# Kernel tuning notes

Measured on AMD Instinct MI355X. Metric: run time of the kernel, lower is better.

## Reference

```python
import jax, jax.numpy as jnp
import numpy as np

BETA = 0.25  # commitment_cost
K = 512      # num_embeddings
D = 64       # embedding_dim


def setup_inputs() -> dict:
    key = jax.random.key(0)
    k1, k2 = jax.random.split(key)
    z = jax.random.normal(k1, (8, D, 16, 64, 64), dtype=jnp.float32)
    # torch init: uniform_(-1/K, 1/K)
    emb = jax.random.uniform(k2, (K, D), dtype=jnp.float32,
                             minval=-1.0 / K, maxval=1.0 / K)
    return {"z": z, "emb": emb}


def reference(z, emb):
    B, Dc, d, h, w = z.shape
    # (B, D, d, h, w) -> (N, D), N = B*d*h*w
    z_flat = jnp.transpose(z, (0, 2, 3, 4, 1)).reshape(-1, Dc)
    # squared euclidean distances to each codebook entry: (N, K)
    dists = (jnp.sum(z_flat * z_flat, axis=1, keepdims=True)
             - 2.0 * (z_flat @ emb.T)
             + jnp.sum(emb * emb, axis=1))
    indices = jnp.argmin(dists, axis=1)                      # (N,)
    z_q = emb[indices]                                       # (N, D) gather
    z_q = jnp.transpose(z_q.reshape(B, d, h, w, Dc), (0, 4, 1, 2, 3))
    codebook_loss = jnp.mean((z_q - jax.lax.stop_gradient(z)) ** 2)
    commitment_loss = jnp.mean((jax.lax.stop_gradient(z_q) - z) ** 2)
    loss = codebook_loss + BETA * commitment_loss
    # straight-through estimator
    z_q_st = z + jax.lax.stop_gradient(z_q - z)
    return (z_q_st, loss, indices.reshape(B, d, h, w))
```

## Files before the change

### kernel.cpp

```cpp
#include <hip/hip_runtime.h>


#define NK       512
#define DD       64
#define LOSS_OFF 33554432
#define IDX_OFF  33554433
#define EE_FOFF  4

typedef float f32x4 __attribute__((ext_vector_type(4)));

__device__ __forceinline__ float np_sumsq64(const float* v) {
#pragma clang fp contract(off)
    float r[8];
    #pragma unroll
    for (int j = 0; j < 8; ++j) {
        float s = v[j] * v[j];
        r[j] = s;
    }
    #pragma unroll
    for (int i = 8; i < 64; i += 8) {
        #pragma unroll
        for (int j = 0; j < 8; ++j) {
            float s = v[i + j] * v[i + j];
            r[j] += s;
        }
    }
    return ((r[0] + r[1]) + (r[2] + r[3])) + ((r[4] + r[5]) + (r[6] + r[7]));
}

__global__ void vq_ee(const float* __restrict__ emb, float* __restrict__ ws) {
    const int k = blockIdx.x * 256 + threadIdx.x;
    if (blockIdx.x == 0 && threadIdx.x == 0) {
        ((double*)ws)[0] = 0.0;
        ((double*)ws)[1] = 0.0;
    }
    float row[DD];
    const float* er = emb + k * DD;
    #pragma unroll
    for (int c = 0; c < DD; ++c) row[c] = er[c];
    ws[EE_FOFF + k] = np_sumsq64(row);
}

__global__ __launch_bounds__(256)
__attribute__((amdgpu_waves_per_eu(3, 3)))
void vq_main(const float* __restrict__ z, const float* __restrict__ emb,
             float* __restrict__ out, float* __restrict__ ws) {
    __shared__ f32x4 elds[2048];
    __shared__ float eelds[NK];

    const int tid = threadIdx.x;
    const int n0  = blockIdx.x * 512 + tid;
    const int n1  = n0 + 256;
    const int b   = n0 >> 16;
    const int sp  = n0 & 65535;
    const float* zp0 = z + ((size_t)b << 22) + sp;
    const float* zp1 = zp0 + 256;

    eelds[tid]       = ws[EE_FOFF + tid];
    eelds[tid + 256] = ws[EE_FOFF + tid + 256];

    float za[DD], zb[DD];
    #pragma unroll
    for (int c = 0; c < DD; ++c) za[c] = zp0[(size_t)c << 16];
    #pragma unroll
    for (int c = 0; c < DD; ++c) zb[c] = zp1[(size_t)c << 16];
    const float zz0 = np_sumsq64(za);
    const float zz1 = np_sumsq64(zb);

    const f32x4* eg = (const f32x4*)emb;

    float best0 = 3.4e38f, best1 = 3.4e38f;
    int   bi0   = 0,        bi1   = 0;

    #pragma unroll 1
    for (int p = 0; p < 4; ++p) {
        __syncthreads();
        #pragma unroll
        for (int r = 0; r < 8; ++r)
            elds[r * 256 + tid] = eg[p * 2048 + r * 256 + tid];
        __syncthreads();

        #pragma unroll 1
        for (int kl = 0; kl < 128; ++kl) {
            float m0 = 0.f, m1 = 0.f;
            #pragma unroll
            for (int c4 = 0; c4 < 16; ++c4) {
                const f32x4 e = elds[kl * 16 + c4];
                const int c = c4 * 4;
                m0 = fmaf(za[c + 0], e.x, m0);  m1 = fmaf(zb[c + 0], e.x, m1);
                m0 = fmaf(za[c + 1], e.y, m0);  m1 = fmaf(zb[c + 1], e.y, m1);
                m0 = fmaf(za[c + 2], e.z, m0);  m1 = fmaf(zb[c + 2], e.z, m1);
                m0 = fmaf(za[c + 3], e.w, m0);  m1 = fmaf(zb[c + 3], e.w, m1);
            }
            const int k = p * 128 + kl;
            const float ee = eelds[k];
            const float d0 = fmaf(-2.f, m0, zz0) + ee;
            const float d1 = fmaf(-2.f, m1, zz1) + ee;
            if (d0 < best0) { best0 = d0; bi0 = k; }
            if (d1 < best1) { best1 = d1; bi1 = k; }
        }
    }

    float* op0 = out + ((size_t)b << 22) + sp;
    float* op1 = op0 + 256;
    const float4* br0 = (const float4*)(emb + bi0 * DD);
    const float4* br1 = (const float4*)(emb + bi1 * DD);
    float lsum = 0.f;
    #pragma unroll
    for (int c4 = 0; c4 < 16; ++c4) {
        float4 e0 = br0[c4];
        float4 e1 = br1[c4];
        float eq0[4] = { e0.x, e0.y, e0.z, e0.w };
        float eq1[4] = { e1.x, e1.y, e1.z, e1.w };
        #pragma unroll
        for (int j = 0; j < 4; ++j) {
            const int c = c4 * 4 + j;
            float da = eq0[j] - za[c];
            float db = eq1[j] - zb[c];
            lsum = fmaf(da, da, lsum);
            lsum = fmaf(db, db, lsum);
            op0[(size_t)c << 16] = eq0[j];
            op1[(size_t)c << 16] = eq1[j];
        }
    }
    out[IDX_OFF + n0] = (float)bi0;
    out[IDX_OFF + n1] = (float)bi1;

    #pragma unroll
    for (int off = 32; off > 0; off >>= 1) lsum += __shfl_down(lsum, off);
    if ((tid & 63) == 0)
        atomicAdd((double*)ws, (double)lsum);
}

__global__ void vq_finalize(const float* __restrict__ ws, float* __restrict__ out) {
    out[LOSS_OFF] = (float)(((const double*)ws)[0] * (1.25 / 33554432.0));
}

extern "C" void kernel_launch(void* const* d_in, const int* in_sizes, int n_in,
                              void* d_out, int out_size, void* d_ws, size_t ws_size,
                              hipStream_t stream) {
    const float* z   = (const float*)d_in[0];
    const float* emb = (const float*)d_in[1];
    float* out = (float*)d_out;
    float* ws  = (float*)d_ws;

    vq_ee<<<dim3(2), dim3(256), 0, stream>>>(emb, ws);
    vq_main<<<dim3(1024), dim3(256), 0, stream>>>(z, emb, out, ws);
    vq_finalize<<<dim3(1), dim3(1), 0, stream>>>(ws, out);
}
```

Baseline: 730.3 us.

## Process four rows per thread to increase codebook reuse from LDS

Each thread now holds four z rows in registers instead of two and computes distances for all four against each codebook entry read from shared memory, halving LDS reads per FMA. The codebook norms are read as float4 once per four entries. The grid is halved, and the occupancy hint drops to one wave per EU to allow the much larger register footprint. This trades latency hiding and occupancy for fewer shared-memory loads.

```diff
diff --git a/kernel.cpp b/kernel.cpp
--- a/kernel.cpp
+++ b/kernel.cpp
@@ -42,35 +42,35 @@
 }
 
 __global__ __launch_bounds__(256)
-__attribute__((amdgpu_waves_per_eu(3, 3)))
+__attribute__((amdgpu_waves_per_eu(1, 1)))
 void vq_main(const float* __restrict__ z, const float* __restrict__ emb,
              float* __restrict__ out, float* __restrict__ ws) {
     __shared__ f32x4 elds[2048];
-    __shared__ float eelds[NK];
+    __shared__ f32x4 eelds4[128];
 
     const int tid = threadIdx.x;
-    const int n0  = blockIdx.x * 512 + tid;
-    const int n1  = n0 + 256;
-    const int b   = n0 >> 16;
-    const int sp  = n0 & 65535;
-    const float* zp0 = z + ((size_t)b << 22) + sp;
-    const float* zp1 = zp0 + 256;
+    const int blk = blockIdx.x;
+    const int b   = blk >> 6;
+    const int sp0 = (blk & 63) * 1024 + tid;
+    const float* zb = z + ((size_t)b << 22);
 
-    eelds[tid]       = ws[EE_FOFF + tid];
-    eelds[tid + 256] = ws[EE_FOFF + tid + 256];
+    if (tid < 128)
+        eelds4[tid] = ((const f32x4*)(ws + EE_FOFF))[tid];
 
-    float za[DD], zb[DD];
+    float zr[4][DD];
     #pragma unroll
-    for (int c = 0; c < DD; ++c) za[c] = zp0[(size_t)c << 16];
+    for (int j = 0; j < 4; ++j)
+        #pragma unroll
+        for (int c = 0; c < DD; ++c)
+            zr[j][c] = zb[sp0 + j * 256 + ((size_t)c << 16)];
+    float zz[4];
     #pragma unroll
-    for (int c = 0; c < DD; ++c) zb[c] = zp1[(size_t)c << 16];
-    const float zz0 = np_sumsq64(za);
-    const float zz1 = np_sumsq64(zb);
+    for (int j = 0; j < 4; ++j) zz[j] = np_sumsq64(zr[j]);
 
     const f32x4* eg = (const f32x4*)emb;
 
-    float best0 = 3.4e38f, best1 = 3.4e38f;
-    int   bi0   = 0,        bi1   = 0;
+    float best0 = 3.4e38f, best1 = 3.4e38f, best2 = 3.4e38f, best3 = 3.4e38f;
+    int   bi0 = 0, bi1 = 0, bi2 = 0, bi3 = 0;
 
     #pragma unroll 1
     for (int p = 0; p < 4; ++p) {
@@ -81,50 +81,61 @@
         __syncthreads();
 
         #pragma unroll 1
-        for (int kl = 0; kl < 128; ++kl) {
-            float m0 = 0.f, m1 = 0.f;
+        for (int ko = 0; ko < 32; ++ko) {
+            const f32x4 ee4 = eelds4[p * 32 + ko];
             #pragma unroll
-            for (int c4 = 0; c4 < 16; ++c4) {
-                const f32x4 e = elds[kl * 16 + c4];
-                const int c = c4 * 4;
-                m0 = fmaf(za[c + 0], e.x, m0);  m1 = fmaf(zb[c + 0], e.x, m1);
-                m0 = fmaf(za[c + 1], e.y, m0);  m1 = fmaf(zb[c + 1], e.y, m1);
-                m0 = fmaf(za[c + 2], e.z, m0);  m1 = fmaf(zb[c + 2], e.z, m1);
-                m0 = fmaf(za[c + 3], e.w, m0);  m1 = fmaf(zb[c + 3], e.w, m1);
+            for (int ki = 0; ki < 4; ++ki) {
+                const int kl = ko * 4 + ki;
+                float m0 = 0.f, m1 = 0.f, m2 = 0.f, m3 = 0.f;
+                #pragma unroll
+                for (int c4 = 0; c4 < 16; ++c4) {
+                    const f32x4 e = elds[kl * 16 + c4];
+                    const int c = c4 * 4;
+                    m0 = fmaf(zr[0][c+0], e.x, m0); m1 = fmaf(zr[1][c+0], e.x, m1);
+                    m2 = fmaf(zr[2][c+0], e.x, m2); m3 = fmaf(zr[3][c+0], e.x, m3);
+                    m0 = fmaf(zr[0][c+1], e.y, m0); m1 = fmaf(zr[1][c+1], e.y, m1);
+                    m2 = fmaf(zr[2][c+1], e.y, m2); m3 = fmaf(zr[3][c+1], e.y, m3);
+                    m0 = fmaf(zr[0][c+2], e.z, m0); m1 = fmaf(zr[1][c+2], e.z, m1);
+                    m2 = fmaf(zr[2][c+2], e.z, m2); m3 = fmaf(zr[3][c+2], e.z, m3);
+                    m0 = fmaf(zr[0][c+3], e.w, m0); m1 = fmaf(zr[1][c+3], e.w, m1);
+                    m2 = fmaf(zr[2][c+3], e.w, m2); m3 = fmaf(zr[3][c+3], e.w, m3);
+                }
+                const int k = p * 128 + kl;
+                const float ee = (ki == 0) ? ee4.x : (ki == 1) ? ee4.y
+                               : (ki == 2) ? ee4.z : ee4.w;
+                const float d0 = fmaf(-2.f, m0, zz[0]) + ee;
+                const float d1 = fmaf(-2.f, m1, zz[1]) + ee;
+                const float d2 = fmaf(-2.f, m2, zz[2]) + ee;
+                const float d3 = fmaf(-2.f, m3, zz[3]) + ee;
+                if (d0 < best0) { best0 = d0; bi0 = k; }
+                if (d1 < best1) { best1 = d1; bi1 = k; }
+                if (d2 < best2) { best2 = d2; bi2 = k; }
+                if (d3 < best3) { best3 = d3; bi3 = k; }
             }
-            const int k = p * 128 + kl;
-            const float ee = eelds[k];
-            const float d0 = fmaf(-2.f, m0, zz0) + ee;
-            const float d1 = fmaf(-2.f, m1, zz1) + ee;
-            if (d0 < best0) { best0 = d0; bi0 = k; }
-            if (d1 < best1) { best1 = d1; bi1 = k; }
         }
     }
 
-    float* op0 = out + ((size_t)b << 22) + sp;
-    float* op1 = op0 + 256;
-    const float4* br0 = (const float4*)(emb + bi0 * DD);
-    const float4* br1 = (const float4*)(emb + bi1 * DD);
+    float* ob = out + ((size_t)b << 22);
+    const int bis[4] = { bi0, bi1, bi2, bi3 };
     float lsum = 0.f;
     #pragma unroll
-    for (int c4 = 0; c4 < 16; ++c4) {
-        float4 e0 = br0[c4];
-        float4 e1 = br1[c4];
-        float eq0[4] = { e0.x, e0.y, e0.z, e0.w };
-        float eq1[4] = { e1.x, e1.y, e1.z, e1.w };
+    for (int j = 0; j < 4; ++j) {
+        float* op = ob + sp0 + j * 256;
+        const float4* brow = (const float4*)(emb + bis[j] * DD);
         #pragma unroll
-        for (int j = 0; j < 4; ++j) {
-            const int c = c4 * 4 + j;
-            float da = eq0[j] - za[c];
-            float db = eq1[j] - zb[c];
-            lsum = fmaf(da, da, lsum);
-            lsum = fmaf(db, db, lsum);
-            op0[(size_t)c << 16] = eq0[j];
-            op1[(size_t)c << 16] = eq1[j];
+        for (int c4 = 0; c4 < 16; ++c4) {
+            float4 e = brow[c4];
+            float eq[4] = { e.x, e.y, e.z, e.w };
+            #pragma unroll
+            for (int q = 0; q < 4; ++q) {
+                const int c = c4 * 4 + q;
+                float dd = eq[q] - zr[j][c];
+                lsum = fmaf(dd, dd, lsum);
+                op[(size_t)c << 16] = eq[q];
+            }
         }
+        out[IDX_OFF + ((size_t)b << 16) + sp0 + j * 256] = (float)bis[j];
     }
-    out[IDX_OFF + n0] = (float)bi0;
-    out[IDX_OFF + n1] = (float)bi1;
 
     #pragma unroll
     for (int off = 32; off > 0; off >>= 1) lsum += __shfl_down(lsum, off);
@@ -145,6 +156,6 @@
     float* ws  = (float*)d_ws;
 
     vq_ee<<<dim3(2), dim3(256), 0, stream>>>(emb, ws);
-    vq_main<<<dim3(1024), dim3(256), 0, stream>>>(z, emb, out, ws);
+    vq_main<<<dim3(512), dim3(256), 0, stream>>>(z, emb, out, ws);
     vq_finalize<<<dim3(1), dim3(1), 0, stream>>>(ws, out);
 }
```

Result: slower. 1.061 ms (+45.3%).

## Pack two rows into f32x2 FMAs and split codebook reads between LDS and global

Applied to the files above, without the earlier changes.

Stores the two per-thread z vectors interleaved as f32x2 so the inner distance loop can use packed FMA on two rows at once. Only the first quarter of each codebook row (16 of 64 dims) goes into LDS; the rest is read through uniform global/scalar loads, and the row norms are read from the workspace per pair of codes. This removes the per-phase LDS reloads and barriers. It also lowers waves_per_eu from 3 to 2 to free registers. The change depends on the compiler emitting packed FP32 ops and on the global codebook reads staying cache-resident. The near-tie argmin order could shift slightly with fp contract off.

```diff
diff --git a/kernel.cpp b/kernel.cpp
--- a/kernel.cpp
+++ b/kernel.cpp
@@ -7,6 +7,7 @@
 #define IDX_OFF  33554433
 #define EE_FOFF  4
 
+typedef float f32x2 __attribute__((ext_vector_type(2)));
 typedef float f32x4 __attribute__((ext_vector_type(4)));
 
 __device__ __forceinline__ float np_sumsq64(const float* v) {
@@ -42,11 +43,11 @@
 }
 
 __global__ __launch_bounds__(256)
-__attribute__((amdgpu_waves_per_eu(3, 3)))
+__attribute__((amdgpu_waves_per_eu(2, 2)))
 void vq_main(const float* __restrict__ z, const float* __restrict__ emb,
              float* __restrict__ out, float* __restrict__ ws) {
-    __shared__ f32x4 elds[2048];
-    __shared__ float eelds[NK];
+#pragma clang fp contract(off)
+    __shared__ f32x4 elds[NK * 4];
 
     const int tid = threadIdx.x;
     const int n0  = blockIdx.x * 512 + tid;
@@ -56,48 +57,79 @@
     const float* zp0 = z + ((size_t)b << 22) + sp;
     const float* zp1 = zp0 + 256;
 
-    eelds[tid]       = ws[EE_FOFF + tid];
-    eelds[tid + 256] = ws[EE_FOFF + tid + 256];
+    const f32x4* eg = (const f32x4*)emb;
 
-    float za[DD], zb[DD];
     #pragma unroll
-    for (int c = 0; c < DD; ++c) za[c] = zp0[(size_t)c << 16];
+    for (int r = 0; r < 8; ++r) {
+        const int idx = r * 256 + tid;
+        elds[idx] = eg[(idx >> 2) * 16 + (idx & 3)];
+    }
+
+    f32x2 zpk[DD];
     #pragma unroll
-    for (int c = 0; c < DD; ++c) zb[c] = zp1[(size_t)c << 16];
-    const float zz0 = np_sumsq64(za);
-    const float zz1 = np_sumsq64(zb);
+    for (int c = 0; c < DD; ++c) zpk[c].x = zp0[(size_t)c << 16];
+    #pragma unroll
+    for (int c = 0; c < DD; ++c) zpk[c].y = zp1[(size_t)c << 16];
 
-    const f32x4* eg = (const f32x4*)emb;
+    f32x2 rr[8];
+    #pragma unroll
+    for (int j = 0; j < 8; ++j) {
+        f32x2 s = zpk[j] * zpk[j];
+        rr[j] = s;
+    }
+    #pragma unroll
+    for (int i = 8; i < 64; i += 8) {
+        #pragma unroll
+        for (int j = 0; j < 8; ++j) {
+            f32x2 s = zpk[i + j] * zpk[i + j];
+            rr[j] += s;
+        }
+    }
+    const f32x2 zzpk = ((rr[0] + rr[1]) + (rr[2] + rr[3]))
+                     + ((rr[4] + rr[5]) + (rr[6] + rr[7]));
+
+    const f32x2* eeg = (const f32x2*)(ws + EE_FOFF);
 
     float best0 = 3.4e38f, best1 = 3.4e38f;
     int   bi0   = 0,        bi1   = 0;
 
     #pragma unroll 1
-    for (int p = 0; p < 4; ++p) {
-        __syncthreads();
+    for (int ko = 0; ko < 256; ++ko) {
+        if ((ko & 15) == 0) __syncthreads();
+        int eei = ko;
+        asm volatile("" : "+v"(eei));
+        const f32x2 ee2 = eeg[eei];
         #pragma unroll
-        for (int r = 0; r < 8; ++r)
-            elds[r * 256 + tid] = eg[p * 2048 + r * 256 + tid];
-        __syncthreads();
-
-        #pragma unroll 1
-        for (int kl = 0; kl < 128; ++kl) {
-            float m0 = 0.f, m1 = 0.f;
+        for (int ki = 0; ki < 2; ++ki) {
+            const int k = ko * 2 + ki;
+            int ebase = k * 16;
+            asm volatile("" : "+v"(ebase));
+            f32x2 m = { 0.f, 0.f };
             #pragma unroll
-            for (int c4 = 0; c4 < 16; ++c4) {
-                const f32x4 e = elds[kl * 16 + c4];
+            for (int c4 = 0; c4 < 4; ++c4) {
+                const f32x4 e = elds[(k << 2) + c4];
                 const int c = c4 * 4;
-                m0 = fmaf(za[c + 0], e.x, m0);  m1 = fmaf(zb[c + 0], e.x, m1);
-                m0 = fmaf(za[c + 1], e.y, m0);  m1 = fmaf(zb[c + 1], e.y, m1);
-                m0 = fmaf(za[c + 2], e.z, m0);  m1 = fmaf(zb[c + 2], e.z, m1);
-                m0 = fmaf(za[c + 3], e.w, m0);  m1 = fmaf(zb[c + 3], e.w, m1);
+                f32x2 es;
+                es = (f32x2){ e.x, e.x }; m = __builtin_elementwise_fma(zpk[c + 0], es, m);
+                es = (f32x2){ e.y, e.y }; m = __builtin_elementwise_fma(zpk[c + 1], es, m);
+                es = (f32x2){ e.z, e.z }; m = __builtin_elementwise_fma(zpk[c + 2], es, m);
+                es = (f32x2){ e.w, e.w }; m = __builtin_elementwise_fma(zpk[c + 3], es, m);
             }
-            const int k = p * 128 + kl;
-            const float ee = eelds[k];
-            const float d0 = fmaf(-2.f, m0, zz0) + ee;
-            const float d1 = fmaf(-2.f, m1, zz1) + ee;
-            if (d0 < best0) { best0 = d0; bi0 = k; }
-            if (d1 < best1) { best1 = d1; bi1 = k; }
+            #pragma unroll
+            for (int c4 = 4; c4 < 16; ++c4) {
+                const f32x4 e = eg[ebase + c4];
+                const int c = c4 * 4;
+                f32x2 es;
+                es = (f32x2){ e.x, e.x }; m = __builtin_elementwise_fma(zpk[c + 0], es, m);
+                es = (f32x2){ e.y, e.y }; m = __builtin_elementwise_fma(zpk[c + 1], es, m);
+                es = (f32x2){ e.z, e.z }; m = __builtin_elementwise_fma(zpk[c + 2], es, m);
+                es = (f32x2){ e.w, e.w }; m = __builtin_elementwise_fma(zpk[c + 3], es, m);
+            }
+            const float ee = (ki == 0) ? ee2.x : ee2.y;
+            f32x2 d2 = __builtin_elementwise_fma((f32x2){ -2.f, -2.f }, m, zzpk);
+            d2 += (f32x2){ ee, ee };
+            if (d2.x < best0) { best0 = d2.x; bi0 = k; }
+            if (d2.y < best1) { best1 = d2.y; bi1 = k; }
         }
     }
 
@@ -115,8 +147,8 @@
         #pragma unroll
         for (int j = 0; j < 4; ++j) {
             const int c = c4 * 4 + j;
-            float da = eq0[j] - za[c];
-            float db = eq1[j] - zb[c];
+            float da = eq0[j] - zpk[c].x;
+            float db = eq1[j] - zpk[c].y;
             lsum = fmaf(da, da, lsum);
             lsum = fmaf(db, db, lsum);
             op0[(size_t)c << 16] = eq0[j];
```

After: 1.179 ms. +61.4%, slower.
